# Kernel tuning notes

Measured on AMD Instinct MI355X. Metric: run time of the kernel, lower is better.

## Reference

```python
import jax, jax.numpy as jnp
import numpy as np

S, T, H, D = 4096, 4096, 16, 64
N_EMBD = H * D

def setup_inputs() -> dict:
    key = jax.random.key(0)
    kq, kk, kv, kw = jax.random.split(key, 4)
    q = jax.random.normal(kq, (S, H, D), dtype=jnp.float32)
    k = jax.random.normal(kk, (T, H, D), dtype=jnp.float32)
    v = jax.random.normal(kv, (T, H, D), dtype=jnp.float32)
    # GPT-2 style init: std = 0.02 / sqrt(2 * n_layer), n_layer = 24
    W_proj = jax.random.normal(kw, (N_EMBD, N_EMBD), dtype=jnp.float32) * (0.02 / np.sqrt(2 * 24))
    return {"q": q, "k": k, "v": v, "W_proj": W_proj}

def reference(q, k, v, W_proj):
    s, h, d = q.shape
    t = k.shape[0]
    # causal bias: mask positions where query index < key index (future keys)
    causal_bias = (jnp.arange(s)[:, None] < jnp.arange(t)[None, :]).astype(jnp.float32) * -10000.0
    scale = 1.0 / jnp.sqrt(jnp.float32(d))
    # [h, s, t] scores in fp32 (matches original .astype(jnp.float32))
    scores = jnp.einsum('shd,thd->hst', q, k).astype(jnp.float32) * scale + causal_bias
    attn = jax.nn.softmax(scores, axis=-1).astype(q.dtype)
    # dropout p=0 / inference -> identity
    out = jnp.einsum('hst,thd->shd', attn, v).reshape(s, h * d)
    # nn.Linear (no bias) vmapped over tokens: y = x @ W.T
    return out @ W_proj.T
```

## Files before the change

### kernel.cpp

```cpp
#include <hip/hip_runtime.h>

#define S_LEN 4096
#define NH 16
#define DH 64
#define NE 1024

typedef __bf16 bf16_t;
typedef __bf16 bf16x8 __attribute__((ext_vector_type(8)));
typedef __bf16 bf16x4 __attribute__((ext_vector_type(4)));
typedef __bf16 bf16x2 __attribute__((ext_vector_type(2)));
typedef float  f32x4  __attribute__((ext_vector_type(4)));

#define QSCALE 0.180336879f

__global__ __launch_bounds__(256) void pack_all(const float* __restrict__ q,
                                                const float* __restrict__ k,
                                                const float* __restrict__ w,
                                                const float* __restrict__ v,
                                                bf16_t* __restrict__ qb,
                                                bf16_t* __restrict__ kb,
                                                bf16_t* __restrict__ wb,
                                                bf16_t* __restrict__ vt) {
    __shared__ bf16_t tile[64][65];
    const int bid = blockIdx.x;
    if (bid < 4096) {
        const int tid = bid * 256 + threadIdx.x;
        const int e = tid * 4;
        const int s = e >> 10;
        const int c = e & (NE - 1);
        const int h = c >> 6;
        const int d = c & (DH - 1);
        const int o = (h * S_LEN + s) * DH + d;
        float4 qv = *(const float4*)(q + e);
        float4 kv = *(const float4*)(k + e);
        bf16x4 qo, ko;
        qo[0] = (bf16_t)(qv.x * QSCALE); qo[1] = (bf16_t)(qv.y * QSCALE);
        qo[2] = (bf16_t)(qv.z * QSCALE); qo[3] = (bf16_t)(qv.w * QSCALE);
        ko[0] = (bf16_t)kv.x; ko[1] = (bf16_t)kv.y; ko[2] = (bf16_t)kv.z; ko[3] = (bf16_t)kv.w;
        *(bf16x4*)(qb + o) = qo;
        *(bf16x4*)(kb + o) = ko;
        if (tid < (NE * NE / 4)) {
            float4 wv = *(const float4*)(w + tid * 4);
            bf16x4 wo;
            wo[0] = (bf16_t)wv.x; wo[1] = (bf16_t)wv.y; wo[2] = (bf16_t)wv.z; wo[3] = (bf16_t)wv.w;
            *(bf16x4*)(wb + tid * 4) = wo;
        }
    } else {
        const int vb = bid - 4096;
        const int h  = vb >> 6;
        const int t0 = (vb & 63) * 64;
        const int r  = threadIdx.x >> 6;
        const int cl = threadIdx.x & 63;
#pragma unroll
        for (int rep = 0; rep < 16; ++rep) {
            int i = rep * 4 + r;
            tile[cl][i] = (bf16_t)v[(t0 + i) * NE + h * DH + cl];
        }
        __syncthreads();
        const int r2  = threadIdx.x >> 5;
        const int cl2 = (threadIdx.x & 31) * 2;
#pragma unroll
        for (int rep = 0; rep < 8; ++rep) {
            int d = rep * 8 + r2;
            bf16x2 out;
            out[0] = tile[d][cl2];
            out[1] = tile[d][cl2 + 1];
            *(bf16x2*)(vt + (h * DH + d) * S_LEN + t0 + cl2) = out;
        }
    }
}

__global__ __launch_bounds__(512, 4) void attn(const bf16_t* __restrict__ qb,
                                               const bf16_t* __restrict__ kb,
                                               const bf16_t* __restrict__ vt,
                                               float* __restrict__ po,
                                               float* __restrict__ ls) {
    __shared__ __align__(16) bf16_t kbuf[2][64 * 72];
    __shared__ __align__(16) bf16_t vbuf[2][64 * 72];

    const int tid  = threadIdx.x;
    const int wave = tid >> 6;
    const int lane = tid & 63;
    const int l15  = lane & 15;
    const int quad = lane >> 4;
    const int h = blockIdx.x;
    const int x = blockIdx.y;

    const int sA = x;
    const int sB = 31 - x;
    const int n0 = x + 1;
    const int b1 = sB + 1;
    const int N  = 33;

    const bf16_t* __restrict__ qh = qb + h * (S_LEN * DH);
    const bf16_t* __restrict__ kh = kb + h * (S_LEN * DH);
    const bf16_t* __restrict__ vh = vt + h * (DH * S_LEN);

    const int row0 = tid >> 3;
    const int tc8  = (tid & 7) * 8;

    f32x4 o_acc[4];
    float lsum;
    bf16x8 qA[2];
    int s0 = sA * 128 + wave * 16;

    auto load_q = [&](int s0_) {
#pragma unroll
        for (int dc = 0; dc < 2; ++dc)
            qA[dc] = *(const bf16x8*)(qh + (s0_ + l15) * DH + dc * 32 + quad * 8);
    };
    auto reset_acc = [&]() {
#pragma unroll
        for (int db = 0; db < 4; ++db) o_acc[db] = (f32x4){0.f, 0.f, 0.f, 0.f};
        lsum = 0.0f;
    };
    auto epilogue = [&](int s0_, int slot) {
        float l2 = lsum;
        l2 += __shfl_xor(l2, 16, 64);
        l2 += __shfl_xor(l2, 32, 64);
        float* poz = po + (size_t)(slot * NH + h) * S_LEN * DH;
#pragma unroll
        for (int db = 0; db < 4; ++db)
#pragma unroll
            for (int r = 0; r < 4; ++r)
                poz[(s0_ + quad * 4 + r) * DH + db * 16 + l15] = o_acc[db][r];
        if (lane < 16) {
            float* lsz = ls + (size_t)(slot * NH + h) * S_LEN;
            lsz[s0_ + lane] = l2;
        }
    };

    load_q(s0);
    reset_acc();

    {
        bf16x8 kr = *(const bf16x8*)(kh + row0 * DH + tc8);
        bf16x8 vr = *(const bf16x8*)(vh + row0 * S_LEN + tc8);
        *(bf16x8*)(kbuf[0] + row0 * 72 + tc8) = kr;
        *(bf16x8*)(vbuf[0] + row0 * 72 + tc8) = vr;
    }
    __syncthreads();

    for (int j = 0; j < N; ++j) {
        if (j == n0) {
            epilogue(s0, 0);
            s0 = sB * 128 + wave * 16;
            load_q(s0);
            reset_acc();
        }
        const int t0 = (j < n0 ? j : b1 + (j - n0)) * 64;
        const bf16_t* kb_ = kbuf[j & 1];
        const bf16_t* vb_ = vbuf[j & 1];

        bf16x8 krn, vrn;
        const bool pf = (j + 1 < N);
        if (pf) {
            const int jn = j + 1;
            const int tn = (jn < n0 ? jn : b1 + (jn - n0)) * 64;
            krn = *(const bf16x8*)(kh + (tn + row0) * DH + tc8);
            vrn = *(const bf16x8*)(vh + row0 * S_LEN + tn + tc8);
        }

        if (t0 <= s0 + 15) {
            f32x4 c_[4];
#pragma unroll
            for (int ch = 0; ch < 4; ++ch) {
                bf16x8 kB0 = *(const bf16x8*)(kb_ + (ch * 16 + l15) * 72 + quad * 8);
                bf16x8 kB1 = *(const bf16x8*)(kb_ + (ch * 16 + l15) * 72 + 32 + quad * 8);
                f32x4 zr = (f32x4){0.f, 0.f, 0.f, 0.f};
                zr = __builtin_amdgcn_mfma_f32_16x16x32_bf16(kB0, qA[0], zr, 0, 0, 0);
                zr = __builtin_amdgcn_mfma_f32_16x16x32_bf16(kB1, qA[1], zr, 0, 0, 0);
                c_[ch] = zr;
            }

            const int query = s0 + l15;
            float p[4][4];
#pragma unroll
            for (int ch = 0; ch < 4; ++ch) {
                if (t0 + ch * 16 <= s0 + 15) {
                    const bool edge = (t0 + ch * 16 + 15 > s0);
#pragma unroll
                    for (int r = 0; r < 4; ++r) {
                        float cc = c_[ch][r];
                        if (edge) {
                            int key = t0 + ch * 16 + quad * 4 + r;
                            if (key > query) cc = -INFINITY;
                        }
                        float pv = exp2f(cc - 17.0f);
                        lsum += pv;
                        p[ch][r] = pv;
                    }
                } else {
#pragma unroll
                    for (int r = 0; r < 4; ++r) p[ch][r] = 0.0f;
                }
            }

            bf16x8 pA[2];
#pragma unroll
            for (int kc = 0; kc < 2; ++kc) {
                bf16x8 t;
                t[0] = (bf16_t)p[2 * kc][0];     t[1] = (bf16_t)p[2 * kc][1];
                t[2] = (bf16_t)p[2 * kc][2];     t[3] = (bf16_t)p[2 * kc][3];
                t[4] = (bf16_t)p[2 * kc + 1][0]; t[5] = (bf16_t)p[2 * kc + 1][1];
                t[6] = (bf16_t)p[2 * kc + 1][2]; t[7] = (bf16_t)p[2 * kc + 1][3];
                pA[kc] = t;
            }

#pragma unroll
            for (int db = 0; db < 4; ++db) {
#pragma unroll
                for (int kc = 0; kc < 2; ++kc) {
                    const bf16_t* vrow = vb_ + (db * 16 + l15) * 72 + kc * 32 + quad * 4;
                    bf16x4 lo = *(const bf16x4*)(vrow);
                    bf16x4 hi = *(const bf16x4*)(vrow + 16);
                    bf16x8 vB = __builtin_shufflevector(lo, hi, 0, 1, 2, 3, 4, 5, 6, 7);
                    o_acc[db] = __builtin_amdgcn_mfma_f32_16x16x32_bf16(pA[kc], vB, o_acc[db], 0, 0, 0);
                }
            }
        }

        if (pf) {
            *(bf16x8*)(kbuf[(j + 1) & 1] + row0 * 72 + tc8) = krn;
            *(bf16x8*)(vbuf[(j + 1) & 1] + row0 * 72 + tc8) = vrn;
        }
        __syncthreads();
    }

    epilogue(s0, 1);
}

__global__ __launch_bounds__(256) void combine(const float* __restrict__ po,
                                               const float* __restrict__ ls,
                                               bf16_t* __restrict__ xb) {
    const int idx = blockIdx.x * 256 + threadIdx.x;
    const int row = idx >> 8;
    const int c   = (idx & 255) * 4;
    const int h   = c >> 6;
    const int d   = c & 63;
    const size_t base0 = (size_t)(h) * S_LEN * DH + row * DH + d;
    const size_t base1 = (size_t)(NH + h) * S_LEN * DH + row * DH + d;
    float4 o0 = *(const float4*)(po + base0);
    float4 o1 = *(const float4*)(po + base1);
    float l = ls[(size_t)h * S_LEN + row] + ls[(size_t)(NH + h) * S_LEN + row];
    float inv = 1.0f / l;
    bf16x4 out;
    out[0] = (bf16_t)((o0.x + o1.x) * inv);
    out[1] = (bf16_t)((o0.y + o1.y) * inv);
    out[2] = (bf16_t)((o0.z + o1.z) * inv);
    out[3] = (bf16_t)((o0.w + o1.w) * inv);
    *(bf16x4*)(xb + (size_t)row * NE + c) = out;
}

__global__ __launch_bounds__(256, 4) void proj(const bf16_t* __restrict__ xb,
                                               const bf16_t* __restrict__ wb,
                                               float* __restrict__ y) {
    __shared__ __align__(16) bf16_t wbuf[2][64 * 72];
    const int tid  = threadIdx.x;
    const int wave = tid >> 6;
    const int lane = tid & 63;
    const int l15  = lane & 15;
    const int quad = lane >> 4;
    const int m0 = blockIdx.x * 64 + wave * 16;
    const int n0 = blockIdx.y * 64;

    const int row0 = tid >> 3;
    const int tc8  = (tid & 7) * 8;

    f32x4 acc[4];
#pragma unroll
    for (int nb = 0; nb < 4; ++nb) acc[nb] = (f32x4){0.f, 0.f, 0.f, 0.f};

    {
        bf16x8 wr0 = *(const bf16x8*)(wb + (n0 + row0) * NE + tc8);
        bf16x8 wr1 = *(const bf16x8*)(wb + (n0 + row0 + 32) * NE + tc8);
        *(bf16x8*)(wbuf[0] + row0 * 72 + tc8) = wr0;
        *(bf16x8*)(wbuf[0] + (row0 + 32) * 72 + tc8) = wr1;
    }
    bf16x8 a[2];
#pragma unroll
    for (int kc = 0; kc < 2; ++kc)
        a[kc] = *(const bf16x8*)(xb + (m0 + l15) * NE + kc * 32 + quad * 8);
    __syncthreads();

    for (int kt = 0; kt < 16; ++kt) {
        const bf16_t* wb_ = wbuf[kt & 1];
        const bool pf = (kt + 1 < 16);
        bf16x8 wr0, wr1, an[2];
        if (pf) {
            const int kn = (kt + 1) * 64;
            wr0 = *(const bf16x8*)(wb + (n0 + row0) * NE + kn + tc8);
            wr1 = *(const bf16x8*)(wb + (n0 + row0 + 32) * NE + kn + tc8);
#pragma unroll
            for (int kc = 0; kc < 2; ++kc)
                an[kc] = *(const bf16x8*)(xb + (m0 + l15) * NE + kn + kc * 32 + quad * 8);
        }

#pragma unroll
        for (int nb = 0; nb < 4; ++nb)
#pragma unroll
            for (int kc = 0; kc < 2; ++kc) {
                bf16x8 b = *(const bf16x8*)(wb_ + (nb * 16 + l15) * 72 + kc * 32 + quad * 8);
                acc[nb] = __builtin_amdgcn_mfma_f32_16x16x32_bf16(a[kc], b, acc[nb], 0, 0, 0);
            }

        if (pf) {
            *(bf16x8*)(wbuf[(kt + 1) & 1] + row0 * 72 + tc8) = wr0;
            *(bf16x8*)(wbuf[(kt + 1) & 1] + (row0 + 32) * 72 + tc8) = wr1;
#pragma unroll
            for (int kc = 0; kc < 2; ++kc) a[kc] = an[kc];
        }
        __syncthreads();
    }

#pragma unroll
    for (int nb = 0; nb < 4; ++nb)
#pragma unroll
        for (int r = 0; r < 4; ++r)
            y[(m0 + quad * 4 + r) * NE + n0 + nb * 16 + l15] = acc[nb][r];
}

extern "C" void kernel_launch(void* const* d_in, const int* in_sizes, int n_in,
                              void* d_out, int out_size, void* d_ws, size_t ws_size,
                              hipStream_t stream) {
    const float* q = (const float*)d_in[0];
    const float* k = (const float*)d_in[1];
    const float* v = (const float*)d_in[2];
    const float* w = (const float*)d_in[3];
    float* y = (float*)d_out;

    bf16_t* ws = (bf16_t*)d_ws;
    bf16_t* qb = ws;
    bf16_t* kb = qb + 4 * 1024 * 1024;
    bf16_t* vt = kb + 4 * 1024 * 1024;
    bf16_t* wb = vt + 4 * 1024 * 1024;
    bf16_t* xb = wb + 1024 * 1024;
    float*  po = (float*)(xb + 4 * 1024 * 1024);
    float*  ls = po + (size_t)2 * NH * S_LEN * DH;

    pack_all<<<dim3(4096 + 1024), dim3(256), 0, stream>>>(q, k, w, v, qb, kb, wb, vt);
    attn<<<dim3(NH, 32), dim3(512), 0, stream>>>(qb, kb, vt, po, ls);
    combine<<<dim3(4096), dim3(256), 0, stream>>>(po, ls, xb);
    proj<<<dim3(S_LEN / 64, NE / 64), dim3(256), 0, stream>>>(xb, wb, y);
}
```

Before: 207.3 us.

## Permute V layout for vector fragment loads and compute row sums via MFMA

```diff
diff --git a/kernel.cpp b/kernel.cpp
--- a/kernel.cpp
+++ b/kernel.cpp
@@ -59,13 +59,14 @@
         __syncthreads();
         const int r2  = threadIdx.x >> 5;
         const int cl2 = (threadIdx.x & 31) * 2;
+        const int np = (cl2 & 32) + ((cl2 >> 2) & 3) * 8 + ((cl2 >> 4) & 1) * 4 + (cl2 & 3);
 #pragma unroll
         for (int rep = 0; rep < 8; ++rep) {
             int d = rep * 8 + r2;
             bf16x2 out;
             out[0] = tile[d][cl2];
             out[1] = tile[d][cl2 + 1];
-            *(bf16x2*)(vt + (h * DH + d) * S_LEN + t0 + cl2) = out;
+            *(bf16x2*)(vt + (h * DH + d) * S_LEN + t0 + np) = out;
         }
     }
 }
@@ -98,10 +99,15 @@
 
     const int row0 = tid >> 3;
     const int tc8  = (tid & 7) * 8;
+    const int stg  = row0 * 72 + tc8;
+    const int frg  = l15 * 72 + quad * 8;
 
     f32x4 o_acc[4];
-    float lsum;
+    f32x4 rs;
     bf16x8 qA[2];
+    bf16x8 ones;
+#pragma unroll
+    for (int e = 0; e < 8; ++e) ones[e] = (bf16_t)1.0f;
     int s0 = sA * 128 + wave * 16;
 
     auto load_q = [&](int s0_) {
@@ -112,21 +118,19 @@
     auto reset_acc = [&]() {
 #pragma unroll
         for (int db = 0; db < 4; ++db) o_acc[db] = (f32x4){0.f, 0.f, 0.f, 0.f};
-        lsum = 0.0f;
+        rs = (f32x4){0.f, 0.f, 0.f, 0.f};
     };
     auto epilogue = [&](int s0_, int slot) {
-        float l2 = lsum;
-        l2 += __shfl_xor(l2, 16, 64);
-        l2 += __shfl_xor(l2, 32, 64);
         float* poz = po + (size_t)(slot * NH + h) * S_LEN * DH;
 #pragma unroll
         for (int db = 0; db < 4; ++db)
 #pragma unroll
             for (int r = 0; r < 4; ++r)
                 poz[(s0_ + quad * 4 + r) * DH + db * 16 + l15] = o_acc[db][r];
-        if (lane < 16) {
+        if (l15 == 0) {
             float* lsz = ls + (size_t)(slot * NH + h) * S_LEN;
-            lsz[s0_ + lane] = l2;
+#pragma unroll
+            for (int r = 0; r < 4; ++r) lsz[s0_ + quad * 4 + r] = rs[r];
         }
     };
 
@@ -136,11 +140,12 @@
     {
         bf16x8 kr = *(const bf16x8*)(kh + row0 * DH + tc8);
         bf16x8 vr = *(const bf16x8*)(vh + row0 * S_LEN + tc8);
-        *(bf16x8*)(kbuf[0] + row0 * 72 + tc8) = kr;
-        *(bf16x8*)(vbuf[0] + row0 * 72 + tc8) = vr;
+        *(bf16x8*)(kbuf[0] + stg) = kr;
+        *(bf16x8*)(vbuf[0] + stg) = vr;
     }
     __syncthreads();
 
+#pragma unroll 2
     for (int j = 0; j < N; ++j) {
         if (j == n0) {
             epilogue(s0, 0);
@@ -165,8 +170,8 @@
             f32x4 c_[4];
 #pragma unroll
             for (int ch = 0; ch < 4; ++ch) {
-                bf16x8 kB0 = *(const bf16x8*)(kb_ + (ch * 16 + l15) * 72 + quad * 8);
-                bf16x8 kB1 = *(const bf16x8*)(kb_ + (ch * 16 + l15) * 72 + 32 + quad * 8);
+                bf16x8 kB0 = *(const bf16x8*)(kb_ + frg + ch * (16 * 72));
+                bf16x8 kB1 = *(const bf16x8*)(kb_ + frg + ch * (16 * 72) + 32);
                 f32x4 zr = (f32x4){0.f, 0.f, 0.f, 0.f};
                 zr = __builtin_amdgcn_mfma_f32_16x16x32_bf16(kB0, qA[0], zr, 0, 0, 0);
                 zr = __builtin_amdgcn_mfma_f32_16x16x32_bf16(kB1, qA[1], zr, 0, 0, 0);
@@ -186,9 +191,7 @@
                             int key = t0 + ch * 16 + quad * 4 + r;
                             if (key > query) cc = -INFINITY;
                         }
-                        float pv = exp2f(cc - 17.0f);
-                        lsum += pv;
-                        p[ch][r] = pv;
+                        p[ch][r] = exp2f(cc);
                     }
                 } else {
 #pragma unroll
@@ -207,22 +210,22 @@
                 pA[kc] = t;
             }
 
+            rs = __builtin_amdgcn_mfma_f32_16x16x32_bf16(pA[0], ones, rs, 0, 0, 0);
+            rs = __builtin_amdgcn_mfma_f32_16x16x32_bf16(pA[1], ones, rs, 0, 0, 0);
+
 #pragma unroll
             for (int db = 0; db < 4; ++db) {
 #pragma unroll
                 for (int kc = 0; kc < 2; ++kc) {
-                    const bf16_t* vrow = vb_ + (db * 16 + l15) * 72 + kc * 32 + quad * 4;
-                    bf16x4 lo = *(const bf16x4*)(vrow);
-                    bf16x4 hi = *(const bf16x4*)(vrow + 16);
-                    bf16x8 vB = __builtin_shufflevector(lo, hi, 0, 1, 2, 3, 4, 5, 6, 7);
+                    bf16x8 vB = *(const bf16x8*)(vb_ + frg + db * (16 * 72) + kc * 32);
                     o_acc[db] = __builtin_amdgcn_mfma_f32_16x16x32_bf16(pA[kc], vB, o_acc[db], 0, 0, 0);
                 }
             }
         }
 
         if (pf) {
-            *(bf16x8*)(kbuf[(j + 1) & 1] + row0 * 72 + tc8) = krn;
-            *(bf16x8*)(vbuf[(j + 1) & 1] + row0 * 72 + tc8) = vrn;
+            *(bf16x8*)(kbuf[(j + 1) & 1] + stg) = krn;
+            *(bf16x8*)(vbuf[(j + 1) & 1] + stg) = vrn;
         }
         __syncthreads();
     }
```

After: 196.3 us. -5.3%, faster.
